# Optimization experiments

Measured on AMD Instinct MI355X. Metric: run time of the kernel, lower is better.

The kernel has to match this reference:

```python
import jax, jax.numpy as jnp
import numpy as np


def setup_inputs() -> dict:
    key = jax.random.key(0)
    ks = jax.random.split(key, 8)
    B, C, N = 4, 256, 4096
    C4 = C // 4
    x = jax.random.normal(ks[0], (B, C, N), dtype=jnp.float32)
    # conv1x1 weights == channel-mixing matrices [out_ch, in_ch]
    Wq = jax.random.normal(ks[1], (C4, C), dtype=jnp.float32) * (1.0 / np.sqrt(C))
    bq = jax.random.normal(ks[2], (C4,), dtype=jnp.float32) * 0.02
    Wk = jax.random.normal(ks[3], (C4, C), dtype=jnp.float32) * (1.0 / np.sqrt(C))
    bk = jax.random.normal(ks[4], (C4,), dtype=jnp.float32) * 0.02
    Wv = jax.random.normal(ks[5], (C, C), dtype=jnp.float32) * (1.0 / np.sqrt(C))
    bv = jax.random.normal(ks[6], (C,), dtype=jnp.float32) * 0.02
    # nn.Parameter(torch.zeros(1)) -> but use nonzero so grads flow through attn path
    gamma = jax.random.normal(ks[7], (1,), dtype=jnp.float32) * 0.1
    return {"x": x, "Wq": Wq, "bq": bq, "Wk": Wk, "bk": bk,
            "Wv": Wv, "bv": bv, "gamma": gamma}


def reference(x, Wq, bq, Wk, bk, Wv, bv, gamma):
    # x: [B, C, N]; conv1x1 == matmul over channel dim
    q = jnp.einsum('oc,bcn->bon', Wq, x) + bq[None, :, None]   # [B, C/4, N]
    k = jnp.einsum('oc,bcn->bon', Wk, x) + bk[None, :, None]   # [B, C/4, N]
    v = jnp.einsum('oc,bcn->bon', Wv, x) + bv[None, :, None]   # [B, C,   N]
    # energy[b, i, j] = <q[:, i], k[:, j]>  (unscaled)
    energy = jnp.einsum('bdi,bdj->bij', q, k)                  # [B, N, N]
    attn = jax.nn.softmax(energy, axis=-1)                     # softmax over j
    # out[b, c, i] = sum_j v[b, c, j] * attn[b, i, j]
    out = jnp.einsum('bcj,bij->bci', v, attn)                  # [B, C, N]
    return gamma[0] * out + x
```

## Files before the change

### kernel.cpp

```cpp
#include <hip/hip_runtime.h>

#define NPTS 4096
#define CDIM 256
#define C4DIM 64

typedef __bf16 bf16x8 __attribute__((ext_vector_type(8)));
typedef float  f32x4  __attribute__((ext_vector_type(4)));

__device__ __forceinline__ void async_cp16(const void* g, void* l) {
    __builtin_amdgcn_global_load_lds(
        (const __attribute__((address_space(1))) void*)g,
        (__attribute__((address_space(3))) void*)l, 16, 0, 0);
}

__global__ __launch_bounds__(256) void wprep_kernel(
    const float* __restrict__ Wq, const float* __restrict__ Wk,
    const float* __restrict__ Wv, __bf16* __restrict__ wsz)
{
    int idx = blockIdx.x * 256 + threadIdx.x;
    int row = idx >> 6;
    int l   = idx & 63;
    const float* src;
    if (row < 64)       src = Wq + (size_t)row * CDIM;
    else if (row < 128) src = Wk + (size_t)(row - 64) * CDIM;
    else                src = Wv + (size_t)(row - 128) * CDIM;
    float4 f = *(const float4*)&src[l * 4];
    int g  = l >> 1;
    int gp = g ^ (row & 7);
    union { __bf16 h[4]; uint2 u; } pk;
    pk.h[0] = (__bf16)f.x; pk.h[1] = (__bf16)f.y;
    pk.h[2] = (__bf16)f.z; pk.h[3] = (__bf16)f.w;
    *(uint2*)&wsz[(size_t)row * CDIM + gp * 8 + (l & 1) * 4] = pk.u;
}

__global__ __launch_bounds__(256, 1) void proj_kernel(
    const float* __restrict__ x,
    const float* __restrict__ bq, const float* __restrict__ bk,
    const float* __restrict__ bv, const __bf16* __restrict__ wsz,
    __bf16* __restrict__ qT, __bf16* __restrict__ kT, __bf16* __restrict__ vo)
{
    __shared__ __align__(16) unsigned char sm[83968];
    auto Xs = (float (*)[65])sm;
    auto OT = (float (*)[68])(sm + 66560);

    const int t    = threadIdx.x;
    const int w    = t >> 6;
    const int lane = t & 63;
    const int quad = lane >> 4;
    const int l16  = lane & 15;

    const int n0 = blockIdx.x * 64;
    const int b  = blockIdx.y;

    #pragma unroll
    for (int s = 0; s < 16; s++) {
        int lin = t + 256 * s;
        int c = lin >> 4, n4 = (lin & 15) * 4;
        *(float4*)&Xs[c][n4] =
            *(const float4*)&x[((size_t)b * CDIM + c) * NPTS + n0 + n4];
    }
    __syncthreads();

    bf16x8 af[8];
    #pragma unroll
    for (int kc = 0; kc < 8; kc++) {
        union { __bf16 h8[8]; bf16x8 v; } pk;
        #pragma unroll
        for (int u = 0; u < 8; u++)
            pk.h8[u] = (__bf16)Xs[kc * 32 + quad * 8 + u][16 * w + l16];
        af[kc] = pk.v;
    }
    __syncthreads();

    const int lhalf = lane >> 5;
    const int rlow  = (2 * w + lhalf) & 7;
    const int slane = ((lane & 31) ^ rlow) * 8;

    #pragma unroll
    for (int s = 0; s < 8; s++)
        async_cp16(wsz + (size_t)(8 * s + 2 * w + lhalf) * CDIM + slane,
                   sm + (s * 4 + w) * 1024);

    f32x4 acc[6][4];
    #pragma unroll
    for (int ot = 0; ot < 6; ot++)
        #pragma unroll
        for (int tc = 0; tc < 4; tc++) acc[ot][tc] = (f32x4)(0.f);

    #pragma unroll
    for (int ot = 0; ot < 6; ot++) {
        __syncthreads();
        if (ot < 5) {
            #pragma unroll
            for (int s = 0; s < 8; s++)
                async_cp16(wsz + (size_t)((ot + 1) * 64 + 8 * s + 2 * w + lhalf) * CDIM + slane,
                           sm + ((ot + 1) & 1) * 32768 + (s * 4 + w) * 1024);
        }
        const unsigned char* Wp = sm + (ot & 1) * 32768;
        #pragma unroll
        for (int kc = 0; kc < 8; kc++) {
            bf16x8 bw[4];
            #pragma unroll
            for (int tc = 0; tc < 4; tc++)
                bw[tc] = *(const bf16x8*)(Wp + (16 * tc + l16) * 512
                                             + (((kc * 4 + quad) ^ (l16 & 7)) << 4));
            #pragma unroll
            for (int tc = 0; tc < 4; tc++)
                acc[ot][tc] = __builtin_amdgcn_mfma_f32_16x16x32_bf16(
                    af[kc], bw[tc], acc[ot][tc], 0, 0, 0);
        }
    }

    #pragma unroll
    for (int ot = 0; ot < 2; ot++) {
        __syncthreads();
        const float* bias = ot ? bk : bq;
        #pragma unroll
        for (int tc = 0; tc < 4; tc++) {
            float bs = bias[16 * tc + l16];
            #pragma unroll
            for (int r4 = 0; r4 < 4; r4++)
                OT[16 * w + 4 * quad + r4][16 * tc + l16] = acc[ot][tc][r4] + bs;
        }
        __syncthreads();
        __bf16* outp = (ot == 0 ? qT : kT) + (size_t)b * NPTS * C4DIM;
        int n = t >> 2, op = (t & 3) * 16;
        union { __bf16 h[16]; uint4 u[2]; } pk;
        #pragma unroll
        for (int u2 = 0; u2 < 16; u2++) pk.h[u2] = (__bf16)OT[n][op + u2];
        *(uint4*)&outp[(size_t)(n0 + n) * C4DIM + op]     = pk.u[0];
        *(uint4*)&outp[(size_t)(n0 + n) * C4DIM + op + 8] = pk.u[1];
    }
    #pragma unroll
    for (int ot = 2; ot < 6; ot++) {
        __syncthreads();
        #pragma unroll
        for (int tc = 0; tc < 4; tc++) {
            float bs = bv[(ot - 2) * 64 + 16 * tc + l16];
            f32x4 v4 = acc[ot][tc];
            v4[0] += bs; v4[1] += bs; v4[2] += bs; v4[3] += bs;
            *(f32x4*)&OT[16 * tc + l16][16 * w + 4 * quad] = v4;
        }
        __syncthreads();
        int cl = t >> 2, np = (t & 3) * 16;
        int ch = (ot - 2) * 64 + cl;
        union { __bf16 h[16]; uint4 u[2]; } pk;
        #pragma unroll
        for (int u2 = 0; u2 < 16; u2++) pk.h[u2] = (__bf16)OT[cl][np + u2];
        __bf16* outp = vo + ((size_t)b * CDIM + ch) * NPTS + n0 + np;
        *(uint4*)&outp[0] = pk.u[0];
        *(uint4*)&outp[8] = pk.u[1];
    }
}

__global__ __launch_bounds__(256, 2) void attn_kernel(
    const __bf16* __restrict__ qT, const __bf16* __restrict__ kT,
    const __bf16* __restrict__ vin, const float* __restrict__ xin,
    const float* __restrict__ gptr, float* __restrict__ out)
{
    __shared__ __align__(16) unsigned char sm[58368];
    unsigned char* Kb = sm;
    unsigned char* Vb = sm + 16384;
    auto Ps  = (__bf16 (*)[72])(sm + 49152);
    auto OTa = (float (*)[68])(sm);
    float* Lp = (float*)(sm + 34816);

    const int t    = threadIdx.x;
    const int w    = t >> 6;
    const int lane = t & 63;
    const int quad = lane >> 4;
    const int l16  = lane & 15;
    const int r    = w >> 1;
    const int jh   = w & 1;

    const int b  = blockIdx.z;
    const int i0 = blockIdx.x * 64;
    const int c0 = blockIdx.y * 128;

    const __bf16* qb = qT  + (size_t)b * NPTS * C4DIM;
    const __bf16* kb = kT  + (size_t)b * NPTS * C4DIM;
    const __bf16* vb = vin + (size_t)b * CDIM * NPTS;

    const int swz = (lane & 7) ^ ((lane >> 3) & 7);
    int koff[2], voff[4];
    #pragma unroll
    for (int s = 0; s < 2; s++) {
        int row = (2 * w + s) * 8 + (lane >> 3);
        koff[s] = row * 128 + swz * 16;
    }
    #pragma unroll
    for (int s = 0; s < 4; s++) {
        int row = (4 * w + s) * 8 + (lane >> 3);
        voff[s] = (c0 + row) * (NPTS * 2) + swz * 16;
    }

    bf16x8 aq[2][2];
    #pragma unroll
    for (int rt = 0; rt < 2; rt++)
        #pragma unroll
        for (int kc = 0; kc < 2; kc++)
            aq[rt][kc] = *(const bf16x8*)&qb[(size_t)(i0 + 32 * r + 16 * rt + l16) * C4DIM
                                             + kc * 32 + quad * 8];

    bf16x8 vone;
    #pragma unroll
    for (int u = 0; u < 8; u++) vone[u] = (__bf16)1.0f;

    f32x4 O[2][8], lacc[2];
    #pragma unroll
    for (int rt = 0; rt < 2; rt++) {
        lacc[rt] = (f32x4)(0.f);
        #pragma unroll
        for (int tc = 0; tc < 8; tc++) O[rt][tc] = (f32x4)(0.f);
    }

    {
        const char* kbase = (const char*)kb;
        const char* vbase = (const char*)vb;
        #pragma unroll
        for (int s = 0; s < 2; s++) async_cp16(kbase + koff[s], Kb + (2 * w + s) * 1024);
        #pragma unroll
        for (int s = 0; s < 4; s++) async_cp16(vbase + voff[s], Vb + (4 * w + s) * 1024);
    }

    int p = 0;
    for (int j0 = 0; j0 < NPTS; j0 += 64, p ^= 1) {
        __syncthreads();

        if (j0 + 64 < NPTS) {
            const char* kbase = (const char*)kb + (size_t)(j0 + 64) * (C4DIM * 2);
            const char* vbase = (const char*)vb + (size_t)(j0 + 64) * 2;
            unsigned char* Kd = Kb + (p ^ 1) * 8192;
            unsigned char* Vd = Vb + (p ^ 1) * 16384;
            #pragma unroll
            for (int s = 0; s < 2; s++) async_cp16(kbase + koff[s], Kd + (2 * w + s) * 1024);
            #pragma unroll
            for (int s = 0; s < 4; s++) async_cp16(vbase + voff[s], Vd + (4 * w + s) * 1024);
        }

        const unsigned char* K = Kb + p * 8192;
        const unsigned char* V = Vb + p * 16384;

        f32x4 S[2][2];
        #pragma unroll
        for (int rt = 0; rt < 2; rt++)
            #pragma unroll
            for (int ct = 0; ct < 2; ct++) S[rt][ct] = (f32x4)(0.f);
        #pragma unroll
        for (int kc = 0; kc < 2; kc++) {
            bf16x8 bk2[2];
            #pragma unroll
            for (int ct = 0; ct < 2; ct++) {
                int row = 32 * jh + 16 * ct + l16;
                int slot = (kc * 4 + quad) ^ (l16 & 7);
                bk2[ct] = *(const bf16x8*)(K + row * 128 + slot * 16);
            }
            #pragma unroll
            for (int rt = 0; rt < 2; rt++)
                #pragma unroll
                for (int ct = 0; ct < 2; ct++)
                    S[rt][ct] = __builtin_amdgcn_mfma_f32_16x16x32_bf16(
                        aq[rt][kc], bk2[ct], S[rt][ct], 0, 0, 0);
        }

        #pragma unroll
        for (int rt = 0; rt < 2; rt++)
            #pragma unroll
            for (int ct = 0; ct < 2; ct++)
                #pragma unroll
                for (int r4 = 0; r4 < 4; r4++)
                    Ps[32 * r + 16 * rt + 4 * quad + r4][32 * jh + 16 * ct + l16] =
                        (__bf16)__expf(S[rt][ct][r4] - 32.0f);

        bf16x8 ap[2];
        #pragma unroll
        for (int rt = 0; rt < 2; rt++)
            ap[rt] = *(const bf16x8*)((const char*)&Ps[32 * r + 16 * rt + l16][0]
                                      + jh * 64 + quad * 16);
        #pragma unroll
        for (int tc = 0; tc < 8; tc++) {
            int row = 16 * tc + l16;
            int slot = (jh * 4 + quad) ^ (l16 & 7);
            bf16x8 bv2 = *(const bf16x8*)(V + row * 128 + slot * 16);
            #pragma unroll
            for (int rt = 0; rt < 2; rt++)
                O[rt][tc] = __builtin_amdgcn_mfma_f32_16x16x32_bf16(
                    ap[rt], bv2, O[rt][tc], 0, 0, 0);
        }
        #pragma unroll
        for (int rt = 0; rt < 2; rt++)
            lacc[rt] = __builtin_amdgcn_mfma_f32_16x16x32_bf16(ap[rt], vone, lacc[rt], 0, 0, 0);
    }

    __syncthreads();
    const float g = gptr[0];

    if (jh == 1) {
        float* dst = (float*)(sm + (size_t)(r * 64 + lane) * 272);
        #pragma unroll
        for (int rt = 0; rt < 2; rt++)
            #pragma unroll
            for (int tc = 0; tc < 8; tc++)
                *(f32x4*)(dst + (rt * 8 + tc) * 4) = O[rt][tc];
        if (l16 == 0) {
            #pragma unroll
            for (int rt = 0; rt < 2; rt++)
                #pragma unroll
                for (int r4 = 0; r4 < 4; r4++)
                    Lp[32 * r + 16 * rt + 4 * quad + r4] = lacc[rt][r4];
        }
    }
    __syncthreads();

    float inv[2][4];
    if (jh == 0) {
        const float* src = (const float*)(sm + (size_t)(r * 64 + lane) * 272);
        #pragma unroll
        for (int rt = 0; rt < 2; rt++)
            #pragma unroll
            for (int tc = 0; tc < 8; tc++)
                O[rt][tc] += *(const f32x4*)(src + (rt * 8 + tc) * 4);
        #pragma unroll
        for (int rt = 0; rt < 2; rt++)
            #pragma unroll
            for (int r4 = 0; r4 < 4; r4++) {
                float ls = lacc[rt][r4] + Lp[32 * r + 16 * rt + 4 * quad + r4];
                inv[rt][r4] = g / ls;
            }
    }
    __syncthreads();

    if (jh == 0) {
        #pragma unroll
        for (int rt = 0; rt < 2; rt++)
            #pragma unroll
            for (int tc = 0; tc < 8; tc++) {
                int c = 16 * tc + l16;
                float4 f;
                f.x = O[rt][tc][0] * inv[rt][0];
                f.y = O[rt][tc][1] * inv[rt][1];
                f.z = O[rt][tc][2] * inv[rt][2];
                f.w = O[rt][tc][3] * inv[rt][3];
                *(float4*)&OTa[c][32 * r + 16 * rt + 4 * quad] = f;
            }
    }
    __syncthreads();

    const float* xb = xin + (size_t)b * CDIM * NPTS;
    float*       ob = out + (size_t)b * CDIM * NPTS;
    #pragma unroll
    for (int s = 0; s < 8; s++) {
        int lin = t + 256 * s;
        int c = lin >> 4, col = (lin & 15) * 4;
        size_t gi = (size_t)(c0 + c) * NPTS + i0 + col;
        float4 ov = *(const float4*)&OTa[c][col];
        float4 xv = *(const float4*)&xb[gi];
        float4 rr;
        rr.x = ov.x + xv.x; rr.y = ov.y + xv.y;
        rr.z = ov.z + xv.z; rr.w = ov.w + xv.w;
        *(float4*)&ob[gi] = rr;
    }
}

extern "C" void kernel_launch(void* const* d_in, const int* in_sizes, int n_in,
                              void* d_out, int out_size, void* d_ws, size_t ws_size,
                              hipStream_t stream) {
    const float* x     = (const float*)d_in[0];
    const float* Wq    = (const float*)d_in[1];
    const float* bq    = (const float*)d_in[2];
    const float* Wk    = (const float*)d_in[3];
    const float* bk    = (const float*)d_in[4];
    const float* Wv    = (const float*)d_in[5];
    const float* bv    = (const float*)d_in[6];
    const float* gamma = (const float*)d_in[7];

    const int B = 4;
    __bf16* qT  = (__bf16*)d_ws;
    __bf16* kT  = qT + (size_t)B * NPTS * C4DIM;
    __bf16* v   = kT + (size_t)B * NPTS * C4DIM;
    __bf16* wsz = v  + (size_t)B * CDIM * NPTS;

    wprep_kernel<<<96, 256, 0, stream>>>(Wq, Wk, Wv, wsz);

    proj_kernel<<<dim3(NPTS/64, B), 256, 0, stream>>>(
        x, bq, bk, bv, wsz, qT, kT, v);

    attn_kernel<<<dim3(NPTS/64, CDIM/128, B), 256, 0, stream>>>(
        qT, kT, v, x, gamma, (float*)d_out);
}
```

Before: 168.9 us.

## Load K fragments straight to registers and halve proj tile for occupancy

The attention kernel stops staging K tiles in LDS. Each wave loads its K fragments directly from global memory into double-buffered registers, prefetching the next tile. The S MFMA operands are swapped so Ps can be written as packed 4-element stores, and the PV MFMAs are wrapped in s_setprio. The projection kernel now handles 32 points per block with 2 blocks per CU and smaller LDS, splitting the output tiles across wave pairs. The aim is to cut LDS traffic and footprint and to raise occupancy, at the cost of more global/L2 loads for K and more register pressure.

```diff
diff --git a/kernel.cpp b/kernel.cpp
--- a/kernel.cpp
+++ b/kernel.cpp
@@ -33,29 +33,30 @@
     *(uint2*)&wsz[(size_t)row * CDIM + gp * 8 + (l & 1) * 4] = pk.u;
 }
 
-__global__ __launch_bounds__(256, 1) void proj_kernel(
+__global__ __launch_bounds__(256, 2) void proj_kernel(
     const float* __restrict__ x,
     const float* __restrict__ bq, const float* __restrict__ bk,
     const float* __restrict__ bv, const __bf16* __restrict__ wsz,
     __bf16* __restrict__ qT, __bf16* __restrict__ kT, __bf16* __restrict__ vo)
 {
-    __shared__ __align__(16) unsigned char sm[83968];
-    auto Xs = (float (*)[65])sm;
-    auto OT = (float (*)[68])(sm + 66560);
+    __shared__ __align__(16) unsigned char sm[65536];
+    auto Xs = (float (*)[33])sm;
 
     const int t    = threadIdx.x;
     const int w    = t >> 6;
     const int lane = t & 63;
     const int quad = lane >> 4;
     const int l16  = lane & 15;
-
-    const int n0 = blockIdx.x * 64;
+    const int nq   = w >> 1;
+    const int th   = w & 1;
+
+    const int n0 = blockIdx.x * 32;
     const int b  = blockIdx.y;
 
     #pragma unroll
-    for (int s = 0; s < 16; s++) {
+    for (int s = 0; s < 8; s++) {
         int lin = t + 256 * s;
-        int c = lin >> 4, n4 = (lin & 15) * 4;
+        int c = lin >> 3, n4 = (lin & 7) * 4;
         *(float4*)&Xs[c][n4] =
             *(const float4*)&x[((size_t)b * CDIM + c) * NPTS + n0 + n4];
     }
@@ -67,7 +68,7 @@
         union { __bf16 h8[8]; bf16x8 v; } pk;
         #pragma unroll
         for (int u = 0; u < 8; u++)
-            pk.h8[u] = (__bf16)Xs[kc * 32 + quad * 8 + u][16 * w + l16];
+            pk.h8[u] = (__bf16)Xs[kc * 32 + quad * 8 + u][16 * nq + l16];
         af[kc] = pk.v;
     }
     __syncthreads();
@@ -81,11 +82,12 @@
         async_cp16(wsz + (size_t)(8 * s + 2 * w + lhalf) * CDIM + slane,
                    sm + (s * 4 + w) * 1024);
 
-    f32x4 acc[6][4];
-    #pragma unroll
-    for (int ot = 0; ot < 6; ot++)
-        #pragma unroll
-        for (int tc = 0; tc < 4; tc++) acc[ot][tc] = (f32x4)(0.f);
+    f32x4 acc[6][2];
+    #pragma unroll
+    for (int ot = 0; ot < 6; ot++) {
+        acc[ot][0] = (f32x4)(0.f);
+        acc[ot][1] = (f32x4)(0.f);
+    }
 
     #pragma unroll
     for (int ot = 0; ot < 6; ot++) {
@@ -99,57 +101,71 @@
         const unsigned char* Wp = sm + (ot & 1) * 32768;
         #pragma unroll
         for (int kc = 0; kc < 8; kc++) {
-            bf16x8 bw[4];
-            #pragma unroll
-            for (int tc = 0; tc < 4; tc++)
-                bw[tc] = *(const bf16x8*)(Wp + (16 * tc + l16) * 512
-                                             + (((kc * 4 + quad) ^ (l16 & 7)) << 4));
-            #pragma unroll
-            for (int tc = 0; tc < 4; tc++)
-                acc[ot][tc] = __builtin_amdgcn_mfma_f32_16x16x32_bf16(
-                    af[kc], bw[tc], acc[ot][tc], 0, 0, 0);
-        }
-    }
-
-    #pragma unroll
-    for (int ot = 0; ot < 2; ot++) {
-        __syncthreads();
-        const float* bias = ot ? bk : bq;
-        #pragma unroll
-        for (int tc = 0; tc < 4; tc++) {
-            float bs = bias[16 * tc + l16];
-            #pragma unroll
-            for (int r4 = 0; r4 < 4; r4++)
-                OT[16 * w + 4 * quad + r4][16 * tc + l16] = acc[ot][tc][r4] + bs;
-        }
-        __syncthreads();
-        __bf16* outp = (ot == 0 ? qT : kT) + (size_t)b * NPTS * C4DIM;
-        int n = t >> 2, op = (t & 3) * 16;
-        union { __bf16 h[16]; uint4 u[2]; } pk;
-        #pragma unroll
-        for (int u2 = 0; u2 < 16; u2++) pk.h[u2] = (__bf16)OT[n][op + u2];
-        *(uint4*)&outp[(size_t)(n0 + n) * C4DIM + op]     = pk.u[0];
-        *(uint4*)&outp[(size_t)(n0 + n) * C4DIM + op + 8] = pk.u[1];
-    }
-    #pragma unroll
-    for (int ot = 2; ot < 6; ot++) {
-        __syncthreads();
-        #pragma unroll
-        for (int tc = 0; tc < 4; tc++) {
-            float bs = bv[(ot - 2) * 64 + 16 * tc + l16];
-            f32x4 v4 = acc[ot][tc];
-            v4[0] += bs; v4[1] += bs; v4[2] += bs; v4[3] += bs;
-            *(f32x4*)&OT[16 * tc + l16][16 * w + 4 * quad] = v4;
-        }
-        __syncthreads();
-        int cl = t >> 2, np = (t & 3) * 16;
-        int ch = (ot - 2) * 64 + cl;
-        union { __bf16 h[16]; uint4 u[2]; } pk;
-        #pragma unroll
-        for (int u2 = 0; u2 < 16; u2++) pk.h[u2] = (__bf16)OT[cl][np + u2];
-        __bf16* outp = vo + ((size_t)b * CDIM + ch) * NPTS + n0 + np;
-        *(uint4*)&outp[0] = pk.u[0];
-        *(uint4*)&outp[8] = pk.u[1];
+            bf16x8 bw[2];
+            #pragma unroll
+            for (int tcl = 0; tcl < 2; tcl++)
+                bw[tcl] = *(const bf16x8*)(Wp + (16 * (2 * th + tcl) + l16) * 512
+                                              + (((kc * 4 + quad) ^ (l16 & 7)) << 4));
+            #pragma unroll
+            for (int tcl = 0; tcl < 2; tcl++)
+                acc[ot][tcl] = __builtin_amdgcn_mfma_f32_16x16x32_bf16(
+                    af[kc], bw[tcl], acc[ot][tcl], 0, 0, 0);
+        }
+    }
+
+    {
+        auto OT = (float (*)[68])sm;
+        #pragma unroll
+        for (int ot = 0; ot < 2; ot++) {
+            __syncthreads();
+            const float* bias = ot ? bk : bq;
+            #pragma unroll
+            for (int tcl = 0; tcl < 2; tcl++) {
+                float bs = bias[16 * (2 * th + tcl) + l16];
+                #pragma unroll
+                for (int r4 = 0; r4 < 4; r4++)
+                    OT[16 * nq + 4 * quad + r4][16 * (2 * th + tcl) + l16] =
+                        acc[ot][tcl][r4] + bs;
+            }
+            __syncthreads();
+            __bf16* outp = (ot == 0 ? qT : kT) + (size_t)b * NPTS * C4DIM;
+            int n = t >> 3, op = (t & 7) * 8;
+            f32x4 o0 = *(const f32x4*)&OT[n][op];
+            f32x4 o1 = *(const f32x4*)&OT[n][op + 4];
+            union { __bf16 h[8]; uint4 u; } pk;
+            #pragma unroll
+            for (int u2 = 0; u2 < 4; u2++) {
+                pk.h[u2]     = (__bf16)o0[u2];
+                pk.h[u2 + 4] = (__bf16)o1[u2];
+            }
+            *(uint4*)&outp[(size_t)(n0 + n) * C4DIM + op] = pk.u;
+        }
+    }
+    {
+        auto OTv = (float (*)[36])sm;
+        #pragma unroll
+        for (int ot = 2; ot < 6; ot++) {
+            __syncthreads();
+            #pragma unroll
+            for (int tcl = 0; tcl < 2; tcl++) {
+                float bs = bv[(ot - 2) * 64 + 16 * (2 * th + tcl) + l16];
+                f32x4 v4 = acc[ot][tcl];
+                v4[0] += bs; v4[1] += bs; v4[2] += bs; v4[3] += bs;
+                *(f32x4*)&OTv[16 * (2 * th + tcl) + l16][16 * nq + 4 * quad] = v4;
+            }
+            __syncthreads();
+            int cl = t >> 2, np = (t & 3) * 8;
+            int ch = (ot - 2) * 64 + cl;
+            f32x4 o0 = *(const f32x4*)&OTv[cl][np];
+            f32x4 o1 = *(const f32x4*)&OTv[cl][np + 4];
+            union { __bf16 h[8]; uint4 u; } pk;
+            #pragma unroll
+            for (int u2 = 0; u2 < 4; u2++) {
+                pk.h[u2]     = (__bf16)o0[u2];
+                pk.h[u2 + 4] = (__bf16)o1[u2];
+            }
+            *(uint4*)&vo[((size_t)b * CDIM + ch) * NPTS + n0 + np] = pk.u;
+        }
     }
 }
 
@@ -158,11 +174,10 @@
     const __bf16* __restrict__ vin, const float* __restrict__ xin,
     const float* __restrict__ gptr, float* __restrict__ out)
 {
-    __shared__ __align__(16) unsigned char sm[58368];
-    unsigned char* Kb = sm;
-    unsigned char* Vb = sm + 16384;
-    auto Ps  = (__bf16 (*)[72])(sm + 49152);
-    auto OTa = (float (*)[68])(sm);
+    __shared__ __align__(16) unsigned char sm[41984];
+    unsigned char* Vb = sm;
+    auto Ps  = (__bf16 (*)[72])(sm + 32768);
+    auto OTa = (float (*)[68])sm;
     float* Lp = (float*)(sm + 34816);
 
     const int t    = threadIdx.x;
@@ -182,12 +197,7 @@
     const __bf16* vb = vin + (size_t)b * CDIM * NPTS;
 
     const int swz = (lane & 7) ^ ((lane >> 3) & 7);
-    int koff[2], voff[4];
-    #pragma unroll
-    for (int s = 0; s < 2; s++) {
-        int row = (2 * w + s) * 8 + (lane >> 3);
-        koff[s] = row * 128 + swz * 16;
-    }
+    int voff[4];
     #pragma unroll
     for (int s = 0; s < 4; s++) {
         int row = (4 * w + s) * 8 + (lane >> 3);
@@ -214,32 +224,37 @@
         for (int tc = 0; tc < 8; tc++) O[rt][tc] = (f32x4)(0.f);
     }
 
+    bf16x8 kr0[2][2], kr1[2][2];
+    #pragma unroll
+    for (int kc = 0; kc < 2; kc++)
+        #pragma unroll
+        for (int ct = 0; ct < 2; ct++)
+            kr0[kc][ct] = *(const bf16x8*)&kb[(size_t)(32 * jh + 16 * ct + l16) * C4DIM
+                                              + kc * 32 + quad * 8];
+
     {
-        const char* kbase = (const char*)kb;
         const char* vbase = (const char*)vb;
         #pragma unroll
-        for (int s = 0; s < 2; s++) async_cp16(kbase + koff[s], Kb + (2 * w + s) * 1024);
-        #pragma unroll
         for (int s = 0; s < 4; s++) async_cp16(vbase + voff[s], Vb + (4 * w + s) * 1024);
     }
 
-    int p = 0;
-    for (int j0 = 0; j0 < NPTS; j0 += 64, p ^= 1) {
+    auto body = [&](int j0, const unsigned char* V, unsigned char* Vd,
+                    bf16x8 (&kcur)[2][2], bf16x8 (&knext)[2][2]) {
         __syncthreads();
 
-        if (j0 + 64 < NPTS) {
-            const char* kbase = (const char*)kb + (size_t)(j0 + 64) * (C4DIM * 2);
-            const char* vbase = (const char*)vb + (size_t)(j0 + 64) * 2;
-            unsigned char* Kd = Kb + (p ^ 1) * 8192;
-            unsigned char* Vd = Vb + (p ^ 1) * 16384;
-            #pragma unroll
-            for (int s = 0; s < 2; s++) async_cp16(kbase + koff[s], Kd + (2 * w + s) * 1024);
+        const int jn = j0 + 64;
+        if (jn < NPTS) {
+            const char* vbase = (const char*)vb + (size_t)jn * 2;
             #pragma unroll
             for (int s = 0; s < 4; s++) async_cp16(vbase + voff[s], Vd + (4 * w + s) * 1024);
         }
-
-        const unsigned char* K = Kb + p * 8192;
-        const unsigned char* V = Vb + p * 16384;
+        const int jk = jn & (NPTS - 1);
+        #pragma unroll
+        for (int kc = 0; kc < 2; kc++)
+            #pragma unroll
+            for (int ct = 0; ct < 2; ct++)
+                knext[kc][ct] = *(const bf16x8*)&kb[(size_t)(jk + 32 * jh + 16 * ct + l16) * C4DIM
+                                                    + kc * 32 + quad * 8];
 
         f32x4 S[2][2];
         #pragma unroll
@@ -247,36 +262,31 @@
             #pragma unroll
             for (int ct = 0; ct < 2; ct++) S[rt][ct] = (f32x4)(0.f);
         #pragma unroll
-        for (int kc = 0; kc < 2; kc++) {
-            bf16x8 bk2[2];
-            #pragma unroll
-            for (int ct = 0; ct < 2; ct++) {
-                int row = 32 * jh + 16 * ct + l16;
-                int slot = (kc * 4 + quad) ^ (l16 & 7);
-                bk2[ct] = *(const bf16x8*)(K + row * 128 + slot * 16);
-            }
+        for (int kc = 0; kc < 2; kc++)
             #pragma unroll
             for (int rt = 0; rt < 2; rt++)
                 #pragma unroll
                 for (int ct = 0; ct < 2; ct++)
                     S[rt][ct] = __builtin_amdgcn_mfma_f32_16x16x32_bf16(
-                        aq[rt][kc], bk2[ct], S[rt][ct], 0, 0, 0);
-        }
-
-        #pragma unroll
-        for (int rt = 0; rt < 2; rt++)
-            #pragma unroll
-            for (int ct = 0; ct < 2; ct++)
+                        kcur[kc][ct], aq[rt][kc], S[rt][ct], 0, 0, 0);
+
+        #pragma unroll
+        for (int rt = 0; rt < 2; rt++)
+            #pragma unroll
+            for (int ct = 0; ct < 2; ct++) {
+                union { __bf16 h[4]; uint2 u; } pk;
                 #pragma unroll
                 for (int r4 = 0; r4 < 4; r4++)
-                    Ps[32 * r + 16 * rt + 4 * quad + r4][32 * jh + 16 * ct + l16] =
-                        (__bf16)__expf(S[rt][ct][r4] - 32.0f);
+                    pk.h[r4] = (__bf16)__expf(S[rt][ct][r4] - 32.0f);
+                *(uint2*)&Ps[32 * r + 16 * rt + l16][32 * jh + 16 * ct + 4 * quad] = pk.u;
+            }
 
         bf16x8 ap[2];
         #pragma unroll
         for (int rt = 0; rt < 2; rt++)
             ap[rt] = *(const bf16x8*)((const char*)&Ps[32 * r + 16 * rt + l16][0]
                                       + jh * 64 + quad * 16);
+        __builtin_amdgcn_s_setprio(1);
         #pragma unroll
         for (int tc = 0; tc < 8; tc++) {
             int row = 16 * tc + l16;
@@ -290,6 +300,12 @@
         #pragma unroll
         for (int rt = 0; rt < 2; rt++)
             lacc[rt] = __builtin_amdgcn_mfma_f32_16x16x32_bf16(ap[rt], vone, lacc[rt], 0, 0, 0);
+        __builtin_amdgcn_s_setprio(0);
+    };
+
+    for (int jj = 0; jj < NPTS; jj += 128) {
+        body(jj,      Vb,         Vb + 16384, kr0, kr1);
+        body(jj + 64, Vb + 16384, Vb,         kr1, kr0);
     }
 
     __syncthreads();
@@ -382,7 +398,7 @@
 
     wprep_kernel<<<96, 256, 0, stream>>>(Wq, Wk, Wv, wsz);
 
-    proj_kernel<<<dim3(NPTS/64, B), 256, 0, stream>>>(
+    proj_kernel<<<dim3(NPTS/32, B), 256, 0, stream>>>(
         x, bq, bk, bv, wsz, qT, kT, v);
 
     attn_kernel<<<dim3(NPTS/64, CDIM/128, B), 256, 0, stream>>>(
```

Result: slower. 176.8 us (+4.7%).
